# Kernel optimization log

Measured on AMD Instinct MI355X. Metric: run time of the kernel, lower is better.

## Reference

```python
import jax, jax.numpy as jnp
import numpy as np

DIM = 4096
N_HEADS = 32
N_KV = 8
HEAD_DIM = 128
WINDOW = 4096
BSZ = 1
SEQ = 2048
REPEATS = N_HEADS // N_KV
SCALE = HEAD_DIM ** -0.5
NEG_INF = -1e9


def setup_inputs() -> dict:
    key = jax.random.key(0)
    ks = jax.random.split(key, 5)
    x = jax.random.normal(ks[0], (1, BSZ, SEQ, DIM), jnp.float32)
    wq = jax.random.normal(ks[1], (N_HEADS * HEAD_DIM, DIM), jnp.float32) * (DIM ** -0.5)
    wk = jax.random.normal(ks[2], (N_KV * HEAD_DIM, DIM), jnp.float32) * (DIM ** -0.5)
    wv = jax.random.normal(ks[3], (N_KV * HEAD_DIM, DIM), jnp.float32) * (DIM ** -0.5)
    wo = jax.random.normal(ks[4], (DIM, N_HEADS * HEAD_DIM), jnp.float32) * (DIM ** -0.5)
    # rotary frequencies (Mistral/LLaMA style, base 10000)
    inv = 1.0 / (10000.0 ** (np.arange(0, HEAD_DIM, 2, dtype=np.float32) / HEAD_DIM))
    ang = np.outer(np.arange(SEQ, dtype=np.float32), inv)  # [SEQ, HEAD_DIM//2]
    freqs_cos = jnp.asarray(np.cos(ang), jnp.float32)
    freqs_sin = jnp.asarray(np.sin(ang), jnp.float32)
    positions = jnp.arange(SEQ, dtype=jnp.int32)
    # sliding-window causal additive mask [SEQ, SEQ]
    i = np.arange(SEQ)[:, None]
    j = np.arange(SEQ)[None, :]
    allowed = (j <= i) & (j > i - WINDOW)
    mask = jnp.asarray(np.where(allowed, 0.0, NEG_INF).astype(np.float32))
    cache_k = jnp.zeros((BSZ, WINDOW, N_KV, HEAD_DIM), jnp.float32)
    cache_v = jnp.zeros((BSZ, WINDOW, N_KV, HEAD_DIM), jnp.float32)
    return dict(x=x, wq=wq, wk=wk, wv=wv, wo=wo, freqs_cos=freqs_cos,
                freqs_sin=freqs_sin, positions=positions, mask=mask,
                cache_k=cache_k, cache_v=cache_v)


def _rope(x, cos, sin):
    # x: [b, s, h, hd]; pairs (x0,x1),(x2,x3),... treated as complex numbers
    xr = x[..., 0::2]
    xi = x[..., 1::2]
    c = cos[None, :, None, :]
    s = sin[None, :, None, :]
    out_r = xr * c - xi * s
    out_i = xr * s + xi * c
    return jnp.stack([out_r, out_i], axis=-1).reshape(x.shape)


def reference(x, wq, wk, wv, wo, freqs_cos, freqs_sin, positions, mask, cache_k, cache_v):
    b, s = BSZ, SEQ
    xf = x.reshape(b, s, DIM)
    xq = (xf @ wq.T).reshape(b, s, N_HEADS, HEAD_DIM)
    xk = (xf @ wk.T).reshape(b, s, N_KV, HEAD_DIM)
    xv = (xf @ wv.T).reshape(b, s, N_KV, HEAD_DIM)
    xq = _rope(xq, freqs_cos, freqs_sin)
    xk = _rope(xk, freqs_cos, freqs_sin)
    # sliding-window KV cache scatter update (last WINDOW positions, mod WINDOW)
    pos = positions[-WINDOW:] % WINDOW
    cache_k = cache_k.at[:, pos].set(xk[:, -WINDOW:])
    cache_v = cache_v.at[:, pos].set(xv[:, -WINDOW:])
    # prefill branch (positions.shape[0] > 1): attend over current xk/xv
    key = jnp.repeat(xk, REPEATS, axis=2)  # GQA repeat_kv -> [b, s, H, hd]
    val = jnp.repeat(xv, REPEATS, axis=2)
    q = xq.transpose(0, 2, 1, 3)  # [b, H, s, hd]
    k = key.transpose(0, 2, 1, 3)
    v = val.transpose(0, 2, 1, 3)
    scores = jnp.einsum('bhqd,bhkd->bhqk', q, k) * SCALE + mask[None, None]
    probs = jax.nn.softmax(scores, axis=-1)
    out = jnp.einsum('bhqk,bhkd->bhqd', probs, v)
    out = out.transpose(0, 2, 1, 3).reshape(1, b, s, N_HEADS * HEAD_DIM)
    return out @ wo.T, cache_k, cache_v
```

## Files before the change

kernel.cpp:

```cpp
#include <hip/hip_runtime.h>
#include <hip/hip_bf16.h>


typedef __attribute__((ext_vector_type(8))) short short8_t;
typedef __attribute__((ext_vector_type(2))) unsigned uint2_t;
typedef __attribute__((ext_vector_type(8))) __bf16 bf16x8;
typedef __attribute__((ext_vector_type(4))) float f32x4;
typedef __attribute__((ext_vector_type(16))) float f32x16;

#define SEQLEN 2048
#define QSCALE 0.08838834764831845f

__device__ __forceinline__ short f2b(float f) {
  if (!__builtin_isfinite(f)) f = 0.0f;
  union { float f; unsigned u; } v; v.f = f;
  unsigned r = (v.u + 0x7fffu + ((v.u >> 16) & 1u)) >> 16;
  return (short)r;
}
__device__ __forceinline__ float sf(float f) {
  return __builtin_isfinite(f) ? f : 0.0f;
}
__device__ __forceinline__ short8_t cvt8(const float* p) {
  f32x4 a = *(const f32x4*)p;
  f32x4 b = *(const f32x4*)(p + 4);
  short8_t o;
  o[0] = f2b(a[0]); o[1] = f2b(a[1]); o[2] = f2b(a[2]); o[3] = f2b(a[3]);
  o[4] = f2b(b[0]); o[5] = f2b(b[1]); o[6] = f2b(b[2]); o[7] = f2b(b[3]);
  return o;
}
__device__ __forceinline__ unsigned pkb(float lo, float hi) {
  union { float f; unsigned u; } a, b; a.f = lo; b.f = hi;
  unsigned ra = (a.u + 0x7fffu + ((a.u >> 16) & 1u)) >> 16;
  unsigned rb = (b.u + 0x7fffu + ((b.u >> 16) & 1u)) & 0xffff0000u;
  return rb | ra;
}

#define GLD16(gp, lp) __builtin_amdgcn_global_load_lds( \
    (const __attribute__((address_space(1))) void*)(gp), \
    (__attribute__((address_space(3))) void*)(lp), 16, 0, 0)

__global__ __launch_bounds__(256) void cvt_bf16(
    const float* __restrict__ in, short* __restrict__ out)
{
  size_t i = ((size_t)blockIdx.x * 256 + threadIdx.x) * 8;
  *(short8_t*)&out[i] = cvt8(in + i);
}

template <int EPI>
__global__ __launch_bounds__(256) void gemm_epi(
    const short* __restrict__ A, const short* __restrict__ W,
    float* __restrict__ C, short* __restrict__ Cb, float* __restrict__ C2,
    const float* __restrict__ fc, const float* __restrict__ fs,
    int K, int ldc)
{
  __shared__ short As[2][128 * 64];
  __shared__ short Ws[2][128 * 64];
  const int tid  = threadIdx.x;
  const int lane = tid & 63;
  const int wid  = tid >> 6;
  const int l15  = lane & 15;
  const int l4   = lane >> 4;

  const int nwg = (int)(gridDim.x * gridDim.y);
  int bid = (int)(blockIdx.y * gridDim.x + blockIdx.x);
  int swz = (bid & 7) * (nwg >> 3) + (bid >> 3);
  const int m0 = (swz / (int)gridDim.x) * 128;
  const int n0 = (swz % (int)gridDim.x) * 128;

  const int wr = (wid >> 1) * 64;
  const int wc = (wid & 1) * 64;
  const int srow = tid >> 3;
  const int scol = (tid & 7) * 8;

  f32x4 acc[4][4] = {};

  const short* Ab = A + (size_t)(m0 + srow) * K + scol;
  const short* Wb = W + (size_t)(n0 + srow) * K + scol;

#pragma unroll
  for (int i = 0; i < 4; ++i) {
    GLD16(Ab + (size_t)(i * 32) * K, &As[0][(i * 32 + wid * 8) * 64]);
    GLD16(Wb + (size_t)(i * 32) * K, &Ws[0][(i * 32 + wid * 8) * 64]);
  }
  __syncthreads();

  int cur = 0;
  for (int k0 = 0; k0 < K; k0 += 64) {
    if (k0 + 64 < K) {
#pragma unroll
      for (int i = 0; i < 4; ++i) {
        GLD16(Ab + (size_t)(i * 32) * K + k0 + 64, &As[cur ^ 1][(i * 32 + wid * 8) * 64]);
        GLD16(Wb + (size_t)(i * 32) * K + k0 + 64, &Ws[cur ^ 1][(i * 32 + wid * 8) * 64]);
      }
    }
#pragma unroll
    for (int kk = 0; kk < 2; ++kk) {
      bf16x8 af[4], wf[4];
#pragma unroll
      for (int m = 0; m < 4; ++m)
        af[m] = *(const bf16x8*)&As[cur][(wr + m * 16 + l15) * 64 + kk * 32 + l4 * 8];
#pragma unroll
      for (int n = 0; n < 4; ++n)
        wf[n] = *(const bf16x8*)&Ws[cur][(wc + n * 16 + l15) * 64 + kk * 32 + l4 * 8];
#pragma unroll
      for (int m = 0; m < 4; ++m)
#pragma unroll
        for (int n = 0; n < 4; ++n)
          acc[m][n] = __builtin_amdgcn_mfma_f32_16x16x32_bf16(af[m], wf[n], acc[m][n], 0, 0, 0);
    }
    __syncthreads();
    cur ^= 1;
  }

#pragma unroll
  for (int m = 0; m < 4; ++m) {
    int rbase = m0 + wr + m * 16 + l4 * 4;
#pragma unroll
    for (int n = 0; n < 4; ++n) {
      int cbase = n0 + wc + n * 16 + l15;
#pragma unroll
      for (int r = 0; r < 4; ++r) {
        float x = acc[m][n][r];
        if (EPI == 0) {
          C[(size_t)(rbase + r) * ldc + cbase] = sf(x);
        } else {
          float xp = __shfl_xor(x, 1, 64);
          int row = rbase + r;
          int p = (cbase & 127) >> 1;
          float c = fc[row * 64 + p], s = fs[row * 64 + p];
          float o = (l15 & 1) ? (xp * s + x * c) : (x * c - xp * s);
          if (EPI == 1) {
            Cb[(size_t)row * 4096 + cbase] = f2b(o * QSCALE);
          } else {
            if (cbase < 1024) {
              C[(size_t)row * 1024 + cbase]  = sf(o);
              Cb[(size_t)row * 1024 + cbase] = f2b(o);
            } else {
              C2[(size_t)row * 1024 + cbase - 1024] = sf(x);
            }
          }
        }
      }
    }
  }
}

__global__ __launch_bounds__(256) void transpose_v(
    const float* __restrict__ cv, short* __restrict__ Vt)
{
  __shared__ short tile[64][72];
  const int t0 = blockIdx.x * 64;
  const int d0 = blockIdx.y * 64;
  const int h  = blockIdx.z;
  const int tid = threadIdx.x;
  const int r = tid >> 3;
  const int c = (tid & 7) * 8;
#pragma unroll
  for (int it = 0; it < 2; ++it) {
    short8_t v = cvt8(&cv[(size_t)(t0 + it * 32 + r) * 1024 + h * 128 + d0 + c]);
    *(short8_t*)&tile[it * 32 + r][c] = v;
  }
  __syncthreads();
#pragma unroll
  for (int it = 0; it < 2; ++it) {
    int dr = it * 32 + r;
    short8_t v;
#pragma unroll
    for (int i = 0; i < 8; ++i) v[i] = tile[c + i][dr];
    *(short8_t*)&Vt[(size_t)(h * 128 + d0 + dr) * SEQLEN + t0 + c] = v;
  }
}

__global__ __launch_bounds__(256) void attn_fwd7(
    const short* __restrict__ Q,
    const short* __restrict__ Kc,
    const short* __restrict__ Vt,
    short* __restrict__ O)
{
  const int bid = (int)blockIdx.x;
  const int kvh = bid & 7;
  const int qt  = 63 - (bid >> 3);
  const int tid = (int)threadIdx.x;
  const int wid = tid >> 6;
  const int h   = kvh * 4 + wid;
  const int lane = tid & 63;
  const int l31 = lane & 31;
  const int hi  = lane >> 5;

  __shared__ short Ks[64 * 128];
  __shared__ short Vs[128 * 64];
  __shared__ short P[4][32][72];
  __shared__ float exch[4][32];

  const int q0 = qt * 32;
  const int qg = q0 + l31;
  const int kend = q0 + 32;

  bf16x8 qf[8];
  {
    const short* qp = Q + (size_t)qg * 4096 + h * 128 + hi * 8;
#pragma unroll
    for (int ks = 0; ks < 8; ++ks) qf[ks] = *(const bf16x8*)(qp + ks * 16);
  }

  f32x16 o0 = {}, o1 = {}, o2 = {}, o3 = {};
  float m = -1e30f, l = 0.f;

  const int krow_base = wid * 16;
  const int vrow_base = wid * 32;
  const int xk = l31 & 15;
  const int xv = l31 & 7;

  for (int kt = 0; kt < kend; kt += 64) {
#pragma unroll
    for (int it = 0; it < 4; ++it) {
      int krow = krow_base + it * 4 + (lane >> 4);
      int kch  = (lane & 15) ^ (krow & 15);
      GLD16(Kc + (size_t)(kt + krow) * 1024 + kvh * 128 + kch * 8,
            &Ks[wid * 2048 + it * 512]);
      int vrow = vrow_base + it * 8 + (lane >> 3);
      int vch  = (lane & 7) ^ (vrow & 7);
      GLD16(Vt + (size_t)(kvh * 128 + vrow) * SEQLEN + kt + vch * 8,
            &Vs[wid * 2048 + it * 512]);
    }
    __syncthreads();

    f32x16 s0 = {}, s1 = {};
    {
      __builtin_amdgcn_s_setprio(1);
#pragma unroll
      for (int ks = 0; ks < 8; ++ks) {
        int ch = (ks * 2 + hi) ^ xk;
        bf16x8 k0 = *(const bf16x8*)&Ks[l31 * 128 + ch * 8];
        bf16x8 k1 = *(const bf16x8*)&Ks[(32 + l31) * 128 + ch * 8];
        s0 = __builtin_amdgcn_mfma_f32_32x32x16_bf16(k0, qf[ks], s0, 0, 0, 0);
        s1 = __builtin_amdgcn_mfma_f32_32x32x16_bf16(k1, qf[ks], s1, 0, 0, 0);
      }
      __builtin_amdgcn_s_setprio(0);
    }

    if (kt + 63 > q0) {
#pragma unroll
      for (int r = 0; r < 16; ++r) {
        int crow = (r & 3) + 8 * (r >> 2) + 4 * hi;
        if (kt + crow > qg)      s0[r] = -1e30f;
        if (kt + 32 + crow > qg) s1[r] = -1e30f;
      }
    }
    {
      float t[8];
#pragma unroll
      for (int r = 0; r < 8; ++r)
        t[r] = fmaxf(fmaxf(s0[r], s0[r + 8]), fmaxf(s1[r], s1[r + 8]));
      float pmax = fmaxf(fmaxf(fmaxf(t[0], t[1]), fmaxf(t[2], t[3])),
                         fmaxf(fmaxf(t[4], t[5]), fmaxf(t[6], t[7])));
      pmax = fmaxf(pmax, __shfl_xor(pmax, 32, 64));
      if (!__all(pmax <= m + 8.f)) {
        float mnew = fmaxf(m, pmax);
        float resc = __expf(m - mnew);
        m = mnew; l *= resc;
        if (lane < 32) exch[wid][l31] = resc;
#pragma unroll
        for (int r = 0; r < 16; ++r) {
          float rs = exch[wid][(r & 3) + 8 * (r >> 2) + 4 * hi];
          o0[r] *= rs; o1[r] *= rs; o2[r] *= rs; o3[r] *= rs;
        }
      }
      float psum = 0.f;
#pragma unroll
      for (int r = 0; r < 16; ++r) { s0[r] = __expf(s0[r] - m); psum += s0[r]; }
#pragma unroll
      for (int r = 0; r < 16; ++r) { s1[r] = __expf(s1[r] - m); psum += s1[r]; }
      l += psum + __shfl_xor(psum, 32, 64);
#pragma unroll
      for (int t4 = 0; t4 < 4; ++t4) {
        int c = 8 * t4 + 4 * hi;
        *(uint2_t*)&P[wid][l31][c]      = uint2_t{pkb(s0[4*t4], s0[4*t4+1]), pkb(s0[4*t4+2], s0[4*t4+3])};
        *(uint2_t*)&P[wid][l31][32 + c] = uint2_t{pkb(s1[4*t4], s1[4*t4+1]), pkb(s1[4*t4+2], s1[4*t4+3])};
      }
    }

#pragma unroll
    for (int g = 0; g < 4; ++g) {
      int ch = (g * 2 + hi) ^ xv;
      bf16x8 vf0 = *(const bf16x8*)&Vs[(l31)      * 64 + ch * 8];
      bf16x8 vf1 = *(const bf16x8*)&Vs[(32 + l31) * 64 + ch * 8];
      bf16x8 vf2 = *(const bf16x8*)&Vs[(64 + l31) * 64 + ch * 8];
      bf16x8 vf3 = *(const bf16x8*)&Vs[(96 + l31) * 64 + ch * 8];
      bf16x8 pf  = *(const bf16x8*)&P[wid][l31][g * 16 + hi * 8];
      __builtin_amdgcn_s_setprio(1);
      o0 = __builtin_amdgcn_mfma_f32_32x32x16_bf16(pf, vf0, o0, 0, 0, 0);
      o1 = __builtin_amdgcn_mfma_f32_32x32x16_bf16(pf, vf1, o1, 0, 0, 0);
      o2 = __builtin_amdgcn_mfma_f32_32x32x16_bf16(pf, vf2, o2, 0, 0, 0);
      o3 = __builtin_amdgcn_mfma_f32_32x32x16_bf16(pf, vf3, o3, 0, 0, 0);
      __builtin_amdgcn_s_setprio(0);
    }
    __syncthreads();
  }

  if (lane < 32) exch[wid][l31] = 1.f / l;
#pragma unroll
  for (int r = 0; r < 16; ++r) {
    int crow = (r & 3) + 8 * (r >> 2) + 4 * hi;
    float inv = exch[wid][crow];
    short* ob = O + (size_t)(q0 + crow) * 4096 + h * 128 + l31;
    ob[0]  = f2b(o0[r] * inv);
    ob[32] = f2b(o1[r] * inv);
    ob[64] = f2b(o2[r] * inv);
    ob[96] = f2b(o3[r] * inv);
  }
}

extern "C" void kernel_launch(void* const* d_in, const int* in_sizes, int n_in,
                              void* d_out, int out_size, void* d_ws, size_t ws_size,
                              hipStream_t stream) {
  const float* x  = (const float*)d_in[0];
  const float* wq = (const float*)d_in[1];
  const float* wk = (const float*)d_in[2];
  const float* wv = (const float*)d_in[3];
  const float* wo = (const float*)d_in[4];
  const float* fc = (const float*)d_in[5];
  const float* fs = (const float*)d_in[6];

  float* out = (float*)d_out;
  float* out_main = out;
  float* cache_k  = out + (size_t)2048 * 4096;
  float* cache_v  = cache_k + (size_t)4096 * 8 * 128;

  short* slotA = (short*)d_ws;
  short* slotB = (short*)((char*)d_ws + 33554432);
  short* Vt    = (short*)((char*)d_ws + 33554432 + 16777216);
  short* x_bf  = slotB;
  short* attn_out = slotB;

  short* q_bf = (short*)out_main;
  short* k_bf = q_bf + (size_t)2048 * 4096;

  cvt_bf16<<<4096, 256, 0, stream>>>(x, x_bf);
  cvt_bf16<<<8192, 256, 0, stream>>>(wq, slotA);
  gemm_epi<1><<<dim3(32, 16), 256, 0, stream>>>(x_bf, slotA, nullptr, q_bf, nullptr, fc, fs, 4096, 0);

  cvt_bf16<<<2048, 256, 0, stream>>>(wk, slotA);
  cvt_bf16<<<2048, 256, 0, stream>>>(wv, slotA + (size_t)1024 * 4096);
  gemm_epi<2><<<dim3(16, 16), 256, 0, stream>>>(x_bf, slotA, cache_k, k_bf, cache_v, fc, fs, 4096, 0);
  transpose_v<<<dim3(32, 2, 8), 256, 0, stream>>>(cache_v, Vt);
  hipMemsetAsync(cache_k + (size_t)2048 * 1024, 0, (size_t)2048 * 1024 * 4, stream);
  hipMemsetAsync(cache_v + (size_t)2048 * 1024, 0, (size_t)2048 * 1024 * 4, stream);

  attn_fwd7<<<512, 256, 0, stream>>>(q_bf, k_bf, Vt, attn_out);

  cvt_bf16<<<8192, 256, 0, stream>>>(wo, slotA);
  gemm_epi<0><<<dim3(32, 16), 256, 0, stream>>>(attn_out, slotA, out_main, nullptr, nullptr, nullptr, nullptr, 4096, 4096);
}
```

Baseline: 450.2 us.

## Fuse Q/K/V projections into one GEMM and drop LDS double buffering

The separate Q and K/V projection GEMMs are merged into a single GEMM over a concatenated 6144-row bf16 weight. It launches 768 workgroups and uses a column-range epilogue that applies RoPE and writes q, the K cache plus bf16 K, and the V cache. Both GEMM kernels switch from a double-buffered LDS prefetch to a single buffer, synchronising before and after each K-step, which halves LDS use but no longer overlaps loads with MFMA. The workspace layout is reorganised as well, with x_bf and q_bf now placed in the output buffer.

```diff
diff --git a/kernel.cpp b/kernel.cpp
--- a/kernel.cpp
+++ b/kernel.cpp
@@ -46,15 +46,12 @@
   *(short8_t*)&out[i] = cvt8(in + i);
 }
 
-template <int EPI>
-__global__ __launch_bounds__(256) void gemm_epi(
+__global__ __launch_bounds__(256) void gemm_bf(
     const short* __restrict__ A, const short* __restrict__ W,
-    float* __restrict__ C, short* __restrict__ Cb, float* __restrict__ C2,
-    const float* __restrict__ fc, const float* __restrict__ fs,
-    int K, int ldc)
+    float* __restrict__ C, int K, int ldc)
 {
-  __shared__ short As[2][128 * 64];
-  __shared__ short Ws[2][128 * 64];
+  __shared__ short As[128 * 64];
+  __shared__ short Ws[128 * 64];
   const int tid  = threadIdx.x;
   const int lane = tid & 63;
   const int wid  = tid >> 6;
@@ -77,31 +74,23 @@
   const short* Ab = A + (size_t)(m0 + srow) * K + scol;
   const short* Wb = W + (size_t)(n0 + srow) * K + scol;
 
-#pragma unroll
-  for (int i = 0; i < 4; ++i) {
-    GLD16(Ab + (size_t)(i * 32) * K, &As[0][(i * 32 + wid * 8) * 64]);
-    GLD16(Wb + (size_t)(i * 32) * K, &Ws[0][(i * 32 + wid * 8) * 64]);
-  }
-  __syncthreads();
-
-  int cur = 0;
   for (int k0 = 0; k0 < K; k0 += 64) {
-    if (k0 + 64 < K) {
-#pragma unroll
-      for (int i = 0; i < 4; ++i) {
-        GLD16(Ab + (size_t)(i * 32) * K + k0 + 64, &As[cur ^ 1][(i * 32 + wid * 8) * 64]);
-        GLD16(Wb + (size_t)(i * 32) * K + k0 + 64, &Ws[cur ^ 1][(i * 32 + wid * 8) * 64]);
-      }
-    }
+#pragma unroll
+    for (int i = 0; i < 4; ++i) {
+      GLD16(Ab + (size_t)(i * 32) * K + k0, &As[(i * 32 + wid * 8) * 64]);
+      GLD16(Wb + (size_t)(i * 32) * K + k0, &Ws[(i * 32 + wid * 8) * 64]);
+    }
+    __syncthreads();
+
 #pragma unroll
     for (int kk = 0; kk < 2; ++kk) {
       bf16x8 af[4], wf[4];
 #pragma unroll
       for (int m = 0; m < 4; ++m)
-        af[m] = *(const bf16x8*)&As[cur][(wr + m * 16 + l15) * 64 + kk * 32 + l4 * 8];
+        af[m] = *(const bf16x8*)&As[(wr + m * 16 + l15) * 64 + kk * 32 + l4 * 8];
 #pragma unroll
       for (int n = 0; n < 4; ++n)
-        wf[n] = *(const bf16x8*)&Ws[cur][(wc + n * 16 + l15) * 64 + kk * 32 + l4 * 8];
+        wf[n] = *(const bf16x8*)&Ws[(wc + n * 16 + l15) * 64 + kk * 32 + l4 * 8];
 #pragma unroll
       for (int m = 0; m < 4; ++m)
 #pragma unroll
@@ -109,7 +98,6 @@
           acc[m][n] = __builtin_amdgcn_mfma_f32_16x16x32_bf16(af[m], wf[n], acc[m][n], 0, 0, 0);
     }
     __syncthreads();
-    cur ^= 1;
   }
 
 #pragma unroll
@@ -119,26 +107,91 @@
     for (int n = 0; n < 4; ++n) {
       int cbase = n0 + wc + n * 16 + l15;
 #pragma unroll
+      for (int r = 0; r < 4; ++r)
+        C[(size_t)(rbase + r) * ldc + cbase] = sf(acc[m][n][r]);
+    }
+  }
+}
+
+__global__ __launch_bounds__(256) void gemm_qkv(
+    const short* __restrict__ A, const short* __restrict__ W,
+    short* __restrict__ qb, float* __restrict__ ck, short* __restrict__ kb,
+    float* __restrict__ cv,
+    const float* __restrict__ fc, const float* __restrict__ fs)
+{
+  __shared__ short As[128 * 64];
+  __shared__ short Ws[128 * 64];
+  const int K = 4096;
+  const int tid  = threadIdx.x;
+  const int lane = tid & 63;
+  const int wid  = tid >> 6;
+  const int l15  = lane & 15;
+  const int l4   = lane >> 4;
+
+  const int nwg = (int)(gridDim.x * gridDim.y);
+  int bid = (int)(blockIdx.y * gridDim.x + blockIdx.x);
+  int swz = (bid & 7) * (nwg >> 3) + (bid >> 3);
+  const int m0 = (swz / (int)gridDim.x) * 128;
+  const int n0 = (swz % (int)gridDim.x) * 128;
+
+  const int wr = (wid >> 1) * 64;
+  const int wc = (wid & 1) * 64;
+  const int srow = tid >> 3;
+  const int scol = (tid & 7) * 8;
+
+  f32x4 acc[4][4] = {};
+
+  const short* Ab = A + (size_t)(m0 + srow) * K + scol;
+  const short* Wb = W + (size_t)(n0 + srow) * K + scol;
+
+  for (int k0 = 0; k0 < K; k0 += 64) {
+#pragma unroll
+    for (int i = 0; i < 4; ++i) {
+      GLD16(Ab + (size_t)(i * 32) * K + k0, &As[(i * 32 + wid * 8) * 64]);
+      GLD16(Wb + (size_t)(i * 32) * K + k0, &Ws[(i * 32 + wid * 8) * 64]);
+    }
+    __syncthreads();
+
+#pragma unroll
+    for (int kk = 0; kk < 2; ++kk) {
+      bf16x8 af[4], wf[4];
+#pragma unroll
+      for (int m = 0; m < 4; ++m)
+        af[m] = *(const bf16x8*)&As[(wr + m * 16 + l15) * 64 + kk * 32 + l4 * 8];
+#pragma unroll
+      for (int n = 0; n < 4; ++n)
+        wf[n] = *(const bf16x8*)&Ws[(wc + n * 16 + l15) * 64 + kk * 32 + l4 * 8];
+#pragma unroll
+      for (int m = 0; m < 4; ++m)
+#pragma unroll
+        for (int n = 0; n < 4; ++n)
+          acc[m][n] = __builtin_amdgcn_mfma_f32_16x16x32_bf16(af[m], wf[n], acc[m][n], 0, 0, 0);
+    }
+    __syncthreads();
+  }
+
+#pragma unroll
+  for (int m = 0; m < 4; ++m) {
+    int rbase = m0 + wr + m * 16 + l4 * 4;
+#pragma unroll
+    for (int n = 0; n < 4; ++n) {
+      int cbase = n0 + wc + n * 16 + l15;
+#pragma unroll
       for (int r = 0; r < 4; ++r) {
         float x = acc[m][n][r];
-        if (EPI == 0) {
-          C[(size_t)(rbase + r) * ldc + cbase] = sf(x);
+        float xp = __shfl_xor(x, 1, 64);
+        int row = rbase + r;
+        int p = (cbase & 127) >> 1;
+        float c = fc[row * 64 + p], s = fs[row * 64 + p];
+        float o = (l15 & 1) ? (xp * s + x * c) : (x * c - xp * s);
+        if (cbase < 4096) {
+          qb[(size_t)row * 4096 + cbase] = f2b(o * QSCALE);
+        } else if (cbase < 5120) {
+          int kc = cbase - 4096;
+          ck[(size_t)row * 1024 + kc] = sf(o);
+          kb[(size_t)row * 1024 + kc] = f2b(o);
         } else {
-          float xp = __shfl_xor(x, 1, 64);
-          int row = rbase + r;
-          int p = (cbase & 127) >> 1;
-          float c = fc[row * 64 + p], s = fs[row * 64 + p];
-          float o = (l15 & 1) ? (xp * s + x * c) : (x * c - xp * s);
-          if (EPI == 1) {
-            Cb[(size_t)row * 4096 + cbase] = f2b(o * QSCALE);
-          } else {
-            if (cbase < 1024) {
-              C[(size_t)row * 1024 + cbase]  = sf(o);
-              Cb[(size_t)row * 1024 + cbase] = f2b(o);
-            } else {
-              C2[(size_t)row * 1024 + cbase - 1024] = sf(x);
-            }
-          }
+          cv[(size_t)row * 1024 + (cbase - 5120)] = sf(x);
         }
       }
     }
@@ -325,30 +378,31 @@
   float* out = (float*)d_out;
   float* out_main = out;
   float* cache_k  = out + (size_t)2048 * 4096;
-  float* cache_v  = cache_k + (size_t)4096 * 8 * 128;
-
-  short* slotA = (short*)d_ws;
-  short* slotB = (short*)((char*)d_ws + 33554432);
-  short* Vt    = (short*)((char*)d_ws + 33554432 + 16777216);
-  short* x_bf  = slotB;
-  short* attn_out = slotB;
-
-  short* q_bf = (short*)out_main;
-  short* k_bf = q_bf + (size_t)2048 * 4096;
+  float* cache_v  = cache_k + (size_t)4096 * 1024;
+
+  short* Wcat  = (short*)d_ws;
+  short* k_bf  = (short*)((char*)d_ws + 50331648);
+  short* Vt    = (short*)d_ws;
+  short* attn_out = (short*)((char*)d_ws + 4194304);
+  short* wo_bf = (short*)((char*)d_ws + 20971520);
+
+  short* x_bf = (short*)out_main;
+  short* q_bf = x_bf + (size_t)2048 * 4096;
 
   cvt_bf16<<<4096, 256, 0, stream>>>(x, x_bf);
-  cvt_bf16<<<8192, 256, 0, stream>>>(wq, slotA);
-  gemm_epi<1><<<dim3(32, 16), 256, 0, stream>>>(x_bf, slotA, nullptr, q_bf, nullptr, fc, fs, 4096, 0);
-
-  cvt_bf16<<<2048, 256, 0, stream>>>(wk, slotA);
-  cvt_bf16<<<2048, 256, 0, stream>>>(wv, slotA + (size_t)1024 * 4096);
-  gemm_epi<2><<<dim3(16, 16), 256, 0, stream>>>(x_bf, slotA, cache_k, k_bf, cache_v, fc, fs, 4096, 0);
+  cvt_bf16<<<8192, 256, 0, stream>>>(wq, Wcat);
+  cvt_bf16<<<2048, 256, 0, stream>>>(wk, Wcat + (size_t)4096 * 4096);
+  cvt_bf16<<<2048, 256, 0, stream>>>(wv, Wcat + (size_t)5120 * 4096);
+
+  gemm_qkv<<<dim3(48, 16), 256, 0, stream>>>(x_bf, Wcat, q_bf, cache_k, k_bf,
+                                             cache_v, fc, fs);
+
   transpose_v<<<dim3(32, 2, 8), 256, 0, stream>>>(cache_v, Vt);
   hipMemsetAsync(cache_k + (size_t)2048 * 1024, 0, (size_t)2048 * 1024 * 4, stream);
   hipMemsetAsync(cache_v + (size_t)2048 * 1024, 0, (size_t)2048 * 1024 * 4, stream);
 
   attn_fwd7<<<512, 256, 0, stream>>>(q_bf, k_bf, Vt, attn_out);
 
-  cvt_bf16<<<8192, 256, 0, stream>>>(wo, slotA);
-  gemm_epi<0><<<dim3(32, 16), 256, 0, stream>>>(attn_out, slotA, out_main, nullptr, nullptr, nullptr, nullptr, 4096, 4096);
-}
+  cvt_bf16<<<8192, 256, 0, stream>>>(wo, wo_bf);
+  gemm_bf<<<dim3(32, 16), 256, 0, stream>>>(attn_out, wo_bf, out_main, 4096, 4096);
+}
```

Result: no change. 453.1 us (+0.7%).
